# Performance work log

Hardware: AMD Instinct MI355X
Metric: run time of the kernel (lower is better)

The kernel has to match this reference:

```python
import jax, jax.numpy as jnp
import numpy as np

MSG_DIM = 100
REG_WEIGHT = 1.0
N_NODES = 100000
N_EDGES = 1000000
D_FEAT = 6
HIDDEN = 300
OUT_DIM = 2


def setup_inputs() -> dict:
    key = jax.random.key(0)
    ks = jax.random.split(key, 10)
    def glorot(k, shape):
        fan_in = shape[0]
        return jax.random.normal(k, shape, dtype=jnp.float32) / jnp.sqrt(jnp.float32(fan_in))
    return {
        "x": jax.random.normal(ks[0], (N_NODES, D_FEAT), dtype=jnp.float32),
        "edge_index": jax.random.randint(ks[1], (2, N_EDGES), 0, N_NODES, dtype=jnp.int64)
            if jax.config.jax_enable_x64 else jax.random.randint(ks[1], (2, N_EDGES), 0, N_NODES, dtype=jnp.int32),
        "y": jax.random.normal(ks[2], (N_NODES, OUT_DIM), dtype=jnp.float32),
        "target": jax.random.normal(ks[3], (N_NODES, OUT_DIM), dtype=jnp.float32),
        "W1": glorot(ks[4], (2 * D_FEAT, HIDDEN)),
        "b1": jnp.zeros((HIDDEN,), dtype=jnp.float32),
        "W2": glorot(ks[5], (HIDDEN, HIDDEN)),
        "b2": jnp.zeros((HIDDEN,), dtype=jnp.float32),
        "W3": glorot(ks[6], (HIDDEN, 2 * MSG_DIM)),
        "b3": jnp.zeros((2 * MSG_DIM,), dtype=jnp.float32),
    }


def reference(x, edge_index, y, target, W1, b1, W2, b2, W3, b3):
    # MAE term: sum |y - target| / n_nodes
    base_loss = jnp.sum(jnp.abs(y - target)) / y.shape[0]
    # Gather sender/receiver node features per edge and concat -> [E, 2*d_feat]
    e = jnp.concatenate([x[edge_index[0]], x[edge_index[1]]], axis=1)
    # edge_model MLP: 2*d_feat -> 300 -> 300 -> 2*msg_dim
    h = jax.nn.relu(e @ W1 + b1)
    h = jax.nn.relu(h @ W2 + b2)
    messages = h @ W3 + b3  # [E, 2*msg_dim]
    mu = messages[:, :MSG_DIM]
    logvar = messages[:, MSG_DIM:]
    kl_reg = jnp.sum(0.5 * (mu * mu + jnp.exp(logvar) - logvar - 1.0)) / messages.shape[0]
    return base_loss + REG_WEIGHT * kl_reg
```

## Files before the change

### kernel.cpp

```cpp
#include <hip/hip_runtime.h>

#define N_NODES 100000
#define N_EDGES 1000000
#define D_FEAT  6
#define HIDDEN  300
#define HID_P   320
#define MSG     100
#define OUTC    200
#define OUTC_P  208
#define MT      64
#define NT_H    (HID_P/16)
#define NT_M    (OUTC_P/16)
#define KS_H    (HID_P/32)

typedef __bf16 bf16_t;
typedef __bf16 bf16x8 __attribute__((ext_vector_type(8)));
typedef __bf16 bf16x4 __attribute__((ext_vector_type(4)));
typedef float  floatx4 __attribute__((ext_vector_type(4)));

#define PREP_BLOCKS 700
#define LOSS_BLOCKS 200
__global__ void prep_kernel(const float* __restrict__ W1, const float* __restrict__ W2,
                            const float* __restrict__ W3, bf16_t* __restrict__ W1P,
                            bf16_t* __restrict__ W2P, bf16_t* __restrict__ W3P,
                            const float* __restrict__ y, const float* __restrict__ t,
                            float* __restrict__ out) {
    if (blockIdx.x >= PREP_BLOCKS) {
        float s = 0.f;
        for (int i = (blockIdx.x - PREP_BLOCKS) * blockDim.x + threadIdx.x;
             i < N_NODES * 2; i += LOSS_BLOCKS * blockDim.x)
            s += fabsf(y[i] - t[i]);
        #pragma unroll
        for (int off = 32; off; off >>= 1) s += __shfl_down(s, off);
        __shared__ float red[4];
        if ((threadIdx.x & 63) == 0) red[threadIdx.x >> 6] = s;
        __syncthreads();
        if (threadIdx.x == 0)
            atomicAdd(out, (red[0] + red[1] + red[2] + red[3]) * (1.0f / N_NODES));
        return;
    }
    const int n1 = NT_H * 512;
    const int n2 = NT_H * KS_H * 512;
    const int n3 = NT_M * KS_H * 512;
    const int total = n1 + n2 + n3;
    for (int id = blockIdx.x * blockDim.x + threadIdx.x; id < total;
         id += PREP_BLOCKS * blockDim.x) {
        if (id < n1) {
            int nt = id >> 9, rem = id & 511, lane = rem >> 3, j = rem & 7;
            int n = nt * 16 + (lane & 15), k = (lane >> 4) * 8 + j;
            float v = (n < HIDDEN && k < 2 * D_FEAT) ? W1[k * HIDDEN + n] : 0.f;
            W1P[id] = (bf16_t)v;
        } else if (id < n1 + n2) {
            int r = id - n1;
            int chunk = r >> 9, rem = r & 511, lane = rem >> 3, j = rem & 7;
            int ks = chunk % KS_H, nt = chunk / KS_H;
            int n = nt * 16 + (lane & 15), k = ks * 32 + (lane >> 4) * 8 + j;
            float v = (n < HIDDEN && k < HIDDEN) ? W2[k * HIDDEN + n] : 0.f;
            W2P[r] = (bf16_t)v;
        } else {
            int r = id - n1 - n2;
            int chunk = r >> 9, rem = r & 511, lane = rem >> 3, j = rem & 7;
            int ks = chunk % KS_H, nt = chunk / KS_H;
            int n = nt * 16 + (lane & 15), k = ks * 32 + (lane >> 4) * 8 + j;
            float v = (n < OUTC && k < HIDDEN) ? W3[k * OUTC + n] : 0.f;
            W3P[r] = (bf16_t)v;
        }
    }
}

__global__ __launch_bounds__(512, 6) void mlp_kernel(
    const float* __restrict__ x, const int* __restrict__ ei,
    const bf16_t* __restrict__ W1P, const bf16_t* __restrict__ W2P,
    const bf16_t* __restrict__ W3P,
    const float* __restrict__ b1, const float* __restrict__ b2,
    const float* __restrict__ b3, float* __restrict__ out) {
    __shared__ __align__(16) bf16_t A1f[4 * 64 * 8];
    __shared__ __align__(16) bf16_t Hf[4 * KS_H * 64 * 8];
    __shared__ float red[8];

    const int tid  = threadIdx.x;
    const int w    = tid >> 6, lane = tid & 63;
    const int q    = lane >> 4, l16 = lane & 15;
    const int cnt_h = (w < 4) ? 3 : 2;
    const int cnt_m = (w >= 3) ? 2 : 1;
    const long e0 = (long)blockIdx.x * MT;

    *(ulong*)&A1f[tid * 4] = 0ul;
    __syncthreads();
    if (tid < 2 * MT) {
        int m = tid >> 1, side = tid & 1;
        int node = ei[(long)side * N_EDGES + e0 + m];
        const float* xr = x + (long)node * D_FEAT;
        int et = m >> 4, ml = m & 15;
        #pragma unroll
        for (int c = 0; c < D_FEAT; c++) {
            int k = side * D_FEAT + c;
            int lp = ml + 16 * (k >> 3);
            A1f[(et * 64 + lp) * 8 + (k & 7)] = (bf16_t)xr[c];
        }
    }
    __syncthreads();

    floatx4 acc1[3][4];
    {
        bf16x8 hb[4];
        #pragma unroll
        for (int e = 0; e < 4; e++)
            hb[e] = *(const bf16x8*)&A1f[(e * 64 + lane) * 8];
        #pragma unroll
        for (int t = 0; t < 3; t++) {
            if (t < cnt_h) {
                bf16x8 wf = *(const bf16x8*)&W1P[((w + 8 * t) * 64 + lane) * 8];
                #pragma unroll
                for (int e = 0; e < 4; e++) {
                    floatx4 z = {0.f, 0.f, 0.f, 0.f};
                    acc1[t][e] = __builtin_amdgcn_mfma_f32_16x16x32_bf16(wf, hb[e], z, 0, 0, 0);
                }
            }
        }
    }
    #pragma unroll
    for (int t = 0; t < 3; t++) {
        if (t < cnt_h) {
            int n0 = (w + 8 * t) * 16 + 4 * q;
            floatx4 bv = (n0 < HIDDEN) ? *(const floatx4*)&b1[n0]
                                       : (floatx4){0.f, 0.f, 0.f, 0.f};
            int ks = n0 >> 5, lp = l16 + 16 * ((n0 >> 3) & 3), j0 = n0 & 7;
            #pragma unroll
            for (int e = 0; e < 4; e++) {
                bf16x4 pk;
                #pragma unroll
                for (int r = 0; r < 4; r++)
                    pk[r] = (bf16_t)fmaxf(acc1[t][e][r] + bv[r], 0.f);
                *(bf16x4*)&Hf[((e * KS_H + ks) * 64 + lp) * 8 + j0] = pk;
            }
        }
    }
    __syncthreads();

    floatx4 acc2[3][4];
    #pragma unroll
    for (int t = 0; t < 3; t++)
        #pragma unroll
        for (int e = 0; e < 4; e++) acc2[t][e] = (floatx4){0.f, 0.f, 0.f, 0.f};
    #pragma unroll 2
    for (int ks = 0; ks < KS_H; ks++) {
        bf16x8 hb[4];
        #pragma unroll
        for (int e = 0; e < 4; e++)
            hb[e] = *(const bf16x8*)&Hf[((e * KS_H + ks) * 64 + lane) * 8];
        #pragma unroll
        for (int t = 0; t < 3; t++) {
            if (t < cnt_h) {
                bf16x8 wf = *(const bf16x8*)&W2P[(((w + 8 * t) * KS_H + ks) * 64 + lane) * 8];
                #pragma unroll
                for (int e = 0; e < 4; e++)
                    acc2[t][e] = __builtin_amdgcn_mfma_f32_16x16x32_bf16(wf, hb[e], acc2[t][e], 0, 0, 0);
            }
        }
    }
    __syncthreads();
    #pragma unroll
    for (int t = 0; t < 3; t++) {
        if (t < cnt_h) {
            int n0 = (w + 8 * t) * 16 + 4 * q;
            floatx4 bv = (n0 < HIDDEN) ? *(const floatx4*)&b2[n0]
                                       : (floatx4){0.f, 0.f, 0.f, 0.f};
            int ks = n0 >> 5, lp = l16 + 16 * ((n0 >> 3) & 3), j0 = n0 & 7;
            #pragma unroll
            for (int e = 0; e < 4; e++) {
                bf16x4 pk;
                #pragma unroll
                for (int r = 0; r < 4; r++)
                    pk[r] = (bf16_t)fmaxf(acc2[t][e][r] + bv[r], 0.f);
                *(bf16x4*)&Hf[((e * KS_H + ks) * 64 + lp) * 8 + j0] = pk;
            }
        }
    }
    __syncthreads();

    floatx4 acc3[2][4];
    #pragma unroll
    for (int t = 0; t < 2; t++)
        #pragma unroll
        for (int e = 0; e < 4; e++) acc3[t][e] = (floatx4){0.f, 0.f, 0.f, 0.f};
    #pragma unroll 2
    for (int ks = 0; ks < KS_H; ks++) {
        bf16x8 hb[4];
        #pragma unroll
        for (int e = 0; e < 4; e++)
            hb[e] = *(const bf16x8*)&Hf[((e * KS_H + ks) * 64 + lane) * 8];
        #pragma unroll
        for (int t = 0; t < 2; t++) {
            if (t < cnt_m) {
                bf16x8 wf = *(const bf16x8*)&W3P[(((w + 5 * t) * KS_H + ks) * 64 + lane) * 8];
                #pragma unroll
                for (int e = 0; e < 4; e++)
                    acc3[t][e] = __builtin_amdgcn_mfma_f32_16x16x32_bf16(wf, hb[e], acc3[t][e], 0, 0, 0);
            }
        }
    }
    float s = 0.f;
    #pragma unroll
    for (int t = 0; t < 2; t++) {
        if (t < cnt_m) {
            int n0 = (w + 5 * t) * 16 + 4 * q;
            if (n0 < OUTC) {
                floatx4 bv = *(const floatx4*)&b3[n0];
                bool is_mu = (n0 < MSG);
                #pragma unroll
                for (int e = 0; e < 4; e++)
                    #pragma unroll
                    for (int r = 0; r < 4; r++) {
                        float v = acc3[t][e][r] + bv[r];
                        if (is_mu) s += 0.5f * v * v;
                        else       s += 0.5f * (__expf(v) - v - 1.f);
                    }
            }
        }
    }
    #pragma unroll
    for (int off = 32; off; off >>= 1) s += __shfl_down(s, off);
    if (lane == 0) red[w] = s;
    __syncthreads();
    if (tid == 0) {
        float t2 = 0.f;
        #pragma unroll
        for (int i = 0; i < 8; i++) t2 += red[i];
        atomicAdd(out, t2 * (1.0f / N_EDGES));
    }
}

extern "C" void kernel_launch(void* const* d_in, const int* in_sizes, int n_in,
                              void* d_out, int out_size, void* d_ws, size_t ws_size,
                              hipStream_t stream) {
    const float* x      = (const float*)d_in[0];
    const int*   ei     = (const int*)d_in[1];
    const float* y      = (const float*)d_in[2];
    const float* target = (const float*)d_in[3];
    const float* W1     = (const float*)d_in[4];
    const float* b1     = (const float*)d_in[5];
    const float* W2     = (const float*)d_in[6];
    const float* b2     = (const float*)d_in[7];
    const float* W3     = (const float*)d_in[8];
    const float* b3     = (const float*)d_in[9];
    float* out = (float*)d_out;

    bf16_t* W1P = (bf16_t*)d_ws;
    bf16_t* W2P = W1P + NT_H * 512;
    bf16_t* W3P = W2P + NT_H * KS_H * 512;

    hipMemsetAsync(d_out, 0, sizeof(float), stream);
    prep_kernel<<<PREP_BLOCKS + LOSS_BLOCKS, 256, 0, stream>>>(
        W1, W2, W3, W1P, W2P, W3P, y, target, out);
    mlp_kernel<<<N_EDGES / MT, 512, 0, stream>>>(x, ei, W1P, W2P, W3P, b1, b2, b3, out);
}
```

Baseline: 458.1 us.

## Rebalance hidden-layer MFMA work evenly across waves with half-tile sharing

Splits the 20 hidden N-tiles across 8 waves as 2.5 tiles each: every wave owns two full tiles and half of a shared tile (either edge-subtiles 0-1 or 2-3), so no wave runs 3 tiles while others run 2. This is meant to remove the load imbalance in layers 1 and 2 that left some waves idle at each barrier. The x gather is also vectorised into float2 loads with packed bf16 stores. The cost is an extra weight fragment load per wave per k-step for the shared tile, and more template code paths.

```diff
diff --git a/kernel.cpp b/kernel.cpp
--- a/kernel.cpp
+++ b/kernel.cpp
@@ -16,6 +16,7 @@
 typedef __bf16 bf16_t;
 typedef __bf16 bf16x8 __attribute__((ext_vector_type(8)));
 typedef __bf16 bf16x4 __attribute__((ext_vector_type(4)));
+typedef __bf16 bf16x2 __attribute__((ext_vector_type(2)));
 typedef float  floatx4 __attribute__((ext_vector_type(4)));
 
 #define PREP_BLOCKS 700
@@ -68,6 +69,76 @@
     }
 }
 
+static __device__ __forceinline__ floatx4 mfma16(bf16x8 a, bf16x8 b, floatx4 c) {
+    return __builtin_amdgcn_mfma_f32_16x16x32_bf16(a, b, c, 0, 0, 0);
+}
+
+template<int PE0, int KSN, int SE>
+__device__ __forceinline__ void gemm_phase(
+    const bf16_t* __restrict__ Wp, const bf16_t* __restrict__ Hsrc, int lane,
+    int ntA, int ntB, int ntP,
+    floatx4 (&aA)[4], floatx4 (&aB)[4], floatx4 (&aP)[2]) {
+    #pragma unroll
+    for (int e = 0; e < 4; e++) {
+        aA[e] = (floatx4){0.f, 0.f, 0.f, 0.f};
+        aB[e] = (floatx4){0.f, 0.f, 0.f, 0.f};
+    }
+    aP[0] = (floatx4){0.f, 0.f, 0.f, 0.f};
+    aP[1] = (floatx4){0.f, 0.f, 0.f, 0.f};
+    #pragma unroll 2
+    for (int ks = 0; ks < KSN; ks++) {
+        const bf16_t* wb = Wp + ks * 512 + lane * 8;
+        bf16x8 wfA = *(const bf16x8*)(wb + ntA * (KSN * 512));
+        bf16x8 wfB = *(const bf16x8*)(wb + ntB * (KSN * 512));
+        bf16x8 wfP = *(const bf16x8*)(wb + ntP * (KSN * 512));
+        const bf16_t* hb = Hsrc + ks * 512 + lane * 8;
+        bf16x8 h0 = *(const bf16x8*)(hb + 0 * SE);
+        aA[0] = mfma16(wfA, h0, aA[0]);
+        aB[0] = mfma16(wfB, h0, aB[0]);
+        if (PE0 == 0) aP[0] = mfma16(wfP, h0, aP[0]);
+        bf16x8 h1 = *(const bf16x8*)(hb + 1 * SE);
+        aA[1] = mfma16(wfA, h1, aA[1]);
+        aB[1] = mfma16(wfB, h1, aB[1]);
+        if (PE0 == 0) aP[1] = mfma16(wfP, h1, aP[1]);
+        bf16x8 h2 = *(const bf16x8*)(hb + 2 * SE);
+        aA[2] = mfma16(wfA, h2, aA[2]);
+        aB[2] = mfma16(wfB, h2, aB[2]);
+        if (PE0 == 2) aP[0] = mfma16(wfP, h2, aP[0]);
+        bf16x8 h3 = *(const bf16x8*)(hb + 3 * SE);
+        aA[3] = mfma16(wfA, h3, aA[3]);
+        aB[3] = mfma16(wfB, h3, aB[3]);
+        if (PE0 == 2) aP[1] = mfma16(wfP, h3, aP[1]);
+    }
+}
+
+template<int NE>
+__device__ __forceinline__ void epi_job(
+    bf16_t* __restrict__ Hf, const float* __restrict__ bias,
+    int nt, int q, int l16, int e0, const floatx4 (&acc)[NE]) {
+    int n0 = nt * 16 + 4 * q;
+    floatx4 bv = (n0 < HIDDEN) ? *(const floatx4*)&bias[n0]
+                               : (floatx4){0.f, 0.f, 0.f, 0.f};
+    int ks = n0 >> 5, lp = l16 + 16 * ((n0 >> 3) & 3), j0 = n0 & 7;
+    #pragma unroll
+    for (int p = 0; p < NE; p++) {
+        bf16x4 pk;
+        #pragma unroll
+        for (int r = 0; r < 4; r++)
+            pk[r] = (bf16_t)fmaxf(acc[p][r] + bv[r], 0.f);
+        *(bf16x4*)&Hf[(((e0 + p) * KS_H + ks) * 64 + lp) * 8 + j0] = pk;
+    }
+}
+
+template<int PE0>
+__device__ __forceinline__ void epi_h(
+    bf16_t* __restrict__ Hf, const float* __restrict__ bias, int q, int l16,
+    int ntA, int ntB, int ntP,
+    const floatx4 (&aA)[4], const floatx4 (&aB)[4], const floatx4 (&aP)[2]) {
+    epi_job<4>(Hf, bias, ntA, q, l16, 0, aA);
+    epi_job<4>(Hf, bias, ntB, q, l16, 0, aB);
+    epi_job<2>(Hf, bias, ntP, q, l16, PE0, aP);
+}
+
 __global__ __launch_bounds__(512, 6) void mlp_kernel(
     const float* __restrict__ x, const int* __restrict__ ei,
     const bf16_t* __restrict__ W1P, const bf16_t* __restrict__ W2P,
@@ -81,104 +152,59 @@
     const int tid  = threadIdx.x;
     const int w    = tid >> 6, lane = tid & 63;
     const int q    = lane >> 4, l16 = lane & 15;
-    const int cnt_h = (w < 4) ? 3 : 2;
-    const int cnt_m = (w >= 3) ? 2 : 1;
     const long e0 = (long)blockIdx.x * MT;
+
+    const int base = (10 * w) >> 2;
+    const int ntA = (w & 1) ? base + 1 : base;
+    const int ntB = (w & 1) ? base + 2 : base + 1;
+    const int ntP = (w & 1) ? base     : base + 2;
 
     *(ulong*)&A1f[tid * 4] = 0ul;
     __syncthreads();
     if (tid < 2 * MT) {
         int m = tid >> 1, side = tid & 1;
         int node = ei[(long)side * N_EDGES + e0 + m];
-        const float* xr = x + (long)node * D_FEAT;
+        const float2* xr = (const float2*)(x + (long)node * D_FEAT);
+        float2 v0 = xr[0], v1 = xr[1], v2 = xr[2];
         int et = m >> 4, ml = m & 15;
-        #pragma unroll
-        for (int c = 0; c < D_FEAT; c++) {
-            int k = side * D_FEAT + c;
-            int lp = ml + 16 * (k >> 3);
-            A1f[(et * 64 + lp) * 8 + (k & 7)] = (bf16_t)xr[c];
-        }
-    }
-    __syncthreads();
-
-    floatx4 acc1[3][4];
-    {
-        bf16x8 hb[4];
-        #pragma unroll
-        for (int e = 0; e < 4; e++)
-            hb[e] = *(const bf16x8*)&A1f[(e * 64 + lane) * 8];
-        #pragma unroll
-        for (int t = 0; t < 3; t++) {
-            if (t < cnt_h) {
-                bf16x8 wf = *(const bf16x8*)&W1P[((w + 8 * t) * 64 + lane) * 8];
-                #pragma unroll
-                for (int e = 0; e < 4; e++) {
-                    floatx4 z = {0.f, 0.f, 0.f, 0.f};
-                    acc1[t][e] = __builtin_amdgcn_mfma_f32_16x16x32_bf16(wf, hb[e], z, 0, 0, 0);
-                }
-            }
-        }
-    }
-    #pragma unroll
-    for (int t = 0; t < 3; t++) {
-        if (t < cnt_h) {
-            int n0 = (w + 8 * t) * 16 + 4 * q;
-            floatx4 bv = (n0 < HIDDEN) ? *(const floatx4*)&b1[n0]
-                                       : (floatx4){0.f, 0.f, 0.f, 0.f};
-            int ks = n0 >> 5, lp = l16 + 16 * ((n0 >> 3) & 3), j0 = n0 & 7;
-            #pragma unroll
-            for (int e = 0; e < 4; e++) {
-                bf16x4 pk;
-                #pragma unroll
-                for (int r = 0; r < 4; r++)
-                    pk[r] = (bf16_t)fmaxf(acc1[t][e][r] + bv[r], 0.f);
-                *(bf16x4*)&Hf[((e * KS_H + ks) * 64 + lp) * 8 + j0] = pk;
-            }
-        }
-    }
-    __syncthreads();
-
-    floatx4 acc2[3][4];
-    #pragma unroll
-    for (int t = 0; t < 3; t++)
-        #pragma unroll
-        for (int e = 0; e < 4; e++) acc2[t][e] = (floatx4){0.f, 0.f, 0.f, 0.f};
-    #pragma unroll 2
-    for (int ks = 0; ks < KS_H; ks++) {
-        bf16x8 hb[4];
-        #pragma unroll
-        for (int e = 0; e < 4; e++)
-            hb[e] = *(const bf16x8*)&Hf[((e * KS_H + ks) * 64 + lane) * 8];
-        #pragma unroll
-        for (int t = 0; t < 3; t++) {
-            if (t < cnt_h) {
-                bf16x8 wf = *(const bf16x8*)&W2P[(((w + 8 * t) * KS_H + ks) * 64 + lane) * 8];
-                #pragma unroll
-                for (int e = 0; e < 4; e++)
-                    acc2[t][e] = __builtin_amdgcn_mfma_f32_16x16x32_bf16(wf, hb[e], acc2[t][e], 0, 0, 0);
-            }
-        }
-    }
-    __syncthreads();
-    #pragma unroll
-    for (int t = 0; t < 3; t++) {
-        if (t < cnt_h) {
-            int n0 = (w + 8 * t) * 16 + 4 * q;
-            floatx4 bv = (n0 < HIDDEN) ? *(const floatx4*)&b2[n0]
-                                       : (floatx4){0.f, 0.f, 0.f, 0.f};
-            int ks = n0 >> 5, lp = l16 + 16 * ((n0 >> 3) & 3), j0 = n0 & 7;
-            #pragma unroll
-            for (int e = 0; e < 4; e++) {
-                bf16x4 pk;
-                #pragma unroll
-                for (int r = 0; r < 4; r++)
-                    pk[r] = (bf16_t)fmaxf(acc2[t][e][r] + bv[r], 0.f);
-                *(bf16x4*)&Hf[((e * KS_H + ks) * 64 + lp) * 8 + j0] = pk;
-            }
-        }
-    }
-    __syncthreads();
-
+        bf16_t* Ab = &A1f[(et * 64 + ml) * 8];
+        if (side == 0) {
+            bf16x4 lo = {(bf16_t)v0.x, (bf16_t)v0.y, (bf16_t)v1.x, (bf16_t)v1.y};
+            *(bf16x4*)&Ab[0] = lo;
+            bf16x2 mid = {(bf16_t)v2.x, (bf16_t)v2.y};
+            *(bf16x2*)&Ab[4] = mid;
+        } else {
+            bf16x2 hi2 = {(bf16_t)v0.x, (bf16_t)v0.y};
+            *(bf16x2*)&Ab[6] = hi2;
+            bf16x4 top = {(bf16_t)v1.x, (bf16_t)v1.y, (bf16_t)v2.x, (bf16_t)v2.y};
+            *(bf16x4*)&A1f[(et * 64 + ml + 16) * 8] = top;
+        }
+    }
+    __syncthreads();
+
+    floatx4 aA[4], aB[4], aP[2];
+
+    if (w & 1) {
+        gemm_phase<2, 1, 512>(W1P, A1f, lane, ntA, ntB, ntP, aA, aB, aP);
+        epi_h<2>(Hf, b1, q, l16, ntA, ntB, ntP, aA, aB, aP);
+    } else {
+        gemm_phase<0, 1, 512>(W1P, A1f, lane, ntA, ntB, ntP, aA, aB, aP);
+        epi_h<0>(Hf, b1, q, l16, ntA, ntB, ntP, aA, aB, aP);
+    }
+    __syncthreads();
+
+    if (w & 1)
+        gemm_phase<2, KS_H, KS_H * 512>(W2P, Hf, lane, ntA, ntB, ntP, aA, aB, aP);
+    else
+        gemm_phase<0, KS_H, KS_H * 512>(W2P, Hf, lane, ntA, ntB, ntP, aA, aB, aP);
+    __syncthreads();
+    if (w & 1)
+        epi_h<2>(Hf, b2, q, l16, ntA, ntB, ntP, aA, aB, aP);
+    else
+        epi_h<0>(Hf, b2, q, l16, ntA, ntB, ntP, aA, aB, aP);
+    __syncthreads();
+
+    const int cnt_m = (w >= 3) ? 2 : 1;
     floatx4 acc3[2][4];
     #pragma unroll
     for (int t = 0; t < 2; t++)
@@ -196,7 +222,7 @@
                 bf16x8 wf = *(const bf16x8*)&W3P[(((w + 5 * t) * KS_H + ks) * 64 + lane) * 8];
                 #pragma unroll
                 for (int e = 0; e < 4; e++)
-                    acc3[t][e] = __builtin_amdgcn_mfma_f32_16x16x32_bf16(wf, hb[e], acc3[t][e], 0, 0, 0);
+                    acc3[t][e] = mfma16(wf, hb[e], acc3[t][e]);
             }
         }
     }
```

New measurement: 443.2 us. -3.3%, faster.
